# Kernel tuning notes

Measured on AMD Instinct MI355X. Metric: run time of the kernel, lower is better.

Reference implementation:

```python
import jax, jax.numpy as jnp
import numpy as np

S, V, H = 32, 16, 8            # hidden_scalars, hidden_vectors, num_heads
N, E = 10000, 100000           # nodes, edges
NRB, RH = 16, 64               # radial basis, radial MLP hidden
TH = S + 3 * V                 # packed irreps width (80)
WNUM = S * S + V * S + S * V + 2 * V * V  # TP weight_numel = 2560


def setup_inputs() -> dict:
    key = jax.random.key(0)
    ks = jax.random.split(key, 16)
    inp = {}
    inp["node_features"] = jax.random.normal(ks[0], (N, TH), jnp.float32)
    inp["edge_index"] = jax.random.randint(ks[1], (2, E), 0, N)
    inp["edge_sh"] = jax.random.normal(ks[2], (E, 4), jnp.float32)
    inp["edge_radial"] = jax.random.uniform(ks[3], (E, NRB), dtype=jnp.float32)
    inp["edge_envelope"] = jax.random.uniform(ks[4], (E,), dtype=jnp.float32)
    # radial MLP
    inp["W1"] = jax.random.normal(ks[5], (NRB, RH), jnp.float32) / np.sqrt(NRB)
    inp["b1"] = jnp.zeros((RH,), jnp.float32)
    inp["W2"] = jax.random.normal(ks[6], (RH, WNUM), jnp.float32) / np.sqrt(RH)
    inp["b2"] = jnp.zeros((WNUM,), jnp.float32)
    # attention query/key nets (scalar channels only)
    inp["Wq"] = jax.random.normal(ks[7], (S, H), jnp.float32) / np.sqrt(S)
    inp["bq"] = jnp.zeros((H,), jnp.float32)
    inp["Wk"] = jax.random.normal(ks[8], (S, H), jnp.float32) / np.sqrt(S)
    inp["bk"] = jnp.zeros((H,), jnp.float32)
    # equivariant linears (per-irrep channel mixing, e3nn style, no bias)
    inp["Wout_s"] = jax.random.normal(ks[9], (S, S), jnp.float32)
    inp["Wout_v"] = jax.random.normal(ks[10], (V, V), jnp.float32)
    inp["Wg_s"] = jax.random.normal(ks[11], (S, S + V), jnp.float32)
    inp["Wg_v"] = jax.random.normal(ks[12], (V, V), jnp.float32)
    # equivariant batch norm params
    inp["bn_ws"] = jnp.ones((S,), jnp.float32)
    inp["bn_bs"] = jnp.zeros((S,), jnp.float32)
    inp["bn_wv"] = jnp.ones((V,), jnp.float32)
    return inp


def _forward(node_features, edge_sh, edge_radial, edge_envelope,
             W1, b1, W2, b2, Wq, bq, Wk, bk,
             Wout_s, Wout_v, Wg_s, Wg_v, bn_ws, bn_bs, bn_wv, src, dst):
    # --- per-edge TP weights from radial MLP -> (E, WNUM), the big tensor ---
    tp_w = jax.nn.silu(edge_radial @ W1 + b1) @ W2 + b2
    offs = np.cumsum([0, S * S, V * S, S * V, V * V, V * V])
    WA = tp_w[:, offs[0]:offs[1]].reshape(-1, S, S)  # 0e x 0e -> 0e
    WB = tp_w[:, offs[1]:offs[2]].reshape(-1, V, S)  # 1o x 1o -> 0e
    WC = tp_w[:, offs[2]:offs[3]].reshape(-1, S, V)  # 0e x 1o -> 1o
    WD = tp_w[:, offs[3]:offs[4]].reshape(-1, V, V)  # 1o x 0e -> 1o
    WE = tp_w[:, offs[4]:offs[5]].reshape(-1, V, V)  # 1o x 1o -> 1o (cross)

    # --- gather source features, split irreps ---
    s_src = node_features[src, :S]                       # (E, S)
    v_src = node_features[src, S:].reshape(-1, V, 3)     # (E, V, 3)
    y0 = edge_sh[:, 0:1]                                 # (E, 1) l=0
    y1 = edge_sh[:, 1:4]                                 # (E, 3) l=1

    a0 = 1.0 / np.sqrt(S + V)       # path normalization, 0e output
    a1 = 1.0 / np.sqrt(S + 2 * V)   # path normalization, 1o output

    dot = (v_src * y1[:, None, :]).sum(-1) / np.sqrt(3.0)          # (E, V)
    msg_s = a0 * (jnp.einsum('es,esk->ek', s_src * y0, WA)
                  + jnp.einsum('ev,evk->ek', dot, WB))             # (E, S)
    crs = jnp.cross(v_src, y1[:, None, :]) / np.sqrt(2.0)          # (E, V, 3)
    msg_v = a1 * (jnp.einsum('es,ec,esk->ekc', s_src, y1, WC)
                  + jnp.einsum('evc,evk->ekc', v_src * y0[:, :, None], WD)
                  + jnp.einsum('evc,evk->ekc', crs, WE))           # (E, V, 3)
    messages = jnp.concatenate([msg_s, msg_v.reshape(-1, 3 * V)], axis=-1)

    # --- scatter-softmax attention over incoming edges per destination ---
    q = node_features[dst, :S] @ Wq + bq                 # (E, H)
    k = msg_s @ Wk + bk                                  # (E, H)
    logits = (q * k).sum(-1) / np.sqrt(H) + jnp.log(edge_envelope + 1e-8)
    mx = jax.ops.segment_max(logits, dst, num_segments=N)
    ex = jnp.exp(logits - mx[dst])
    den = jax.ops.segment_sum(ex, dst, num_segments=N)
    attn = ex / (den[dst] + 1e-8)                        # (E,)

    agg = jax.ops.segment_sum(attn[:, None] * messages, dst, num_segments=N)

    # --- equivariant output linear ---
    agg_s = agg[:, :S] @ Wout_s / np.sqrt(S)
    agg_v = jnp.einsum('nvc,vw->nwc', agg[:, S:].reshape(-1, V, 3), Wout_v) / np.sqrt(V)

    # --- gate ---
    gs = agg_s @ Wg_s / np.sqrt(S)                       # (N, S+V)
    gv = jnp.einsum('nvc,vw->nwc', agg_v, Wg_v) / np.sqrt(V)
    s = jax.nn.silu(gs[:, :S])
    g = jax.nn.sigmoid(gs[:, S:])
    v = g[:, :, None] * gv
    act = jnp.concatenate([s, v.reshape(-1, 3 * V)], axis=-1)

    # --- residual + equivariant batch norm ---
    x = act + node_features
    xs = x[:, :S]
    xv = x[:, S:].reshape(-1, V, 3)
    mean = xs.mean(0)
    var = xs.var(0)
    xs = (xs - mean) / jnp.sqrt(var + 1e-5) * bn_ws + bn_bs
    vn = (xv * xv).mean(-1).mean(0)                      # (V,) component norm
    xv = xv * (bn_wv / jnp.sqrt(vn + 1e-5))[None, :, None]
    return jnp.concatenate([xs, xv.reshape(-1, 3 * V)], axis=-1)


def reference(node_features, edge_index, edge_sh, edge_radial, edge_envelope,
              W1, b1, W2, b2, Wq, bq, Wk, bk,
              Wout_s, Wout_v, Wg_s, Wg_v, bn_ws, bn_bs, bn_wv):
    src, dst = edge_index[0], edge_index[1]
    return _forward(node_features, edge_sh, edge_radial, edge_envelope,
                    W1, b1, W2, b2, Wq, bq, Wk, bk,
                    Wout_s, Wout_v, Wg_s, Wg_v, bn_ws, bn_bs, bn_wv, src, dst)
```

## Files before the change

### kernel.cpp

```cpp
#include <hip/hip_runtime.h>
#include <math.h>

typedef __bf16 bf16x8 __attribute__((ext_vector_type(8)));
typedef __bf16 bf16x4 __attribute__((ext_vector_type(4)));
typedef float  f32x4  __attribute__((ext_vector_type(4)));
typedef float  f32x2  __attribute__((ext_vector_type(2)));
typedef unsigned long long u64x2 __attribute__((ext_vector_type(2)));

__device__ __forceinline__ float silu_f(float x){ return x / (1.f + __expf(-x)); }
__device__ __forceinline__ float sigm_f(float x){ return 1.f / (1.f + __expf(-x)); }

__device__ __forceinline__ float ntld_f(const float* p){
  return __builtin_nontemporal_load(p);
}
__device__ __forceinline__ float ntbf(const __bf16* p){
  unsigned short us = __builtin_nontemporal_load((const unsigned short*)p);
  union { unsigned u; float f; } cv; cv.u = ((unsigned)us) << 16;
  return cv.f;
}
__device__ __forceinline__ void nt_store_f(float* p, float v){
  __builtin_nontemporal_store(v, p);
}
__device__ __forceinline__ void nt_store_b8(__bf16* p, bf16x8 v){
  u64x2 u; __builtin_memcpy(&u, &v, 16);
// ... 142 lines not shown
  for (int i = t; i < 5120; i += 256){
    int e = i / 80, idx = i - e*80;
    featT[idx][e] = nf[(size_t)src_l[e]*80 + idx];
  }
  for (int i = t; i < 4096; i += 256){
    int e = i & 63, h = i >> 6;
    float acc = b1l[h];
    #pragma unroll
    for (int r = 0; r < 16; ++r) acc += radl[e][r]*w1l[r*64+h];
    u_l[e][h] = (__bf16)silu_f(acc);
  }
  __syncthreads();

  const float inv_s3 = 0.57735026918962576f;
  const float inv_s2 = 0.70710678118654752f;
  const float a0 = 0.14433756729740643f;
  const float a1 = 0.125f;

  for (int i = t; i < 3072; i += 256){
    int r = i >> 6, e = i & 63;
    float val;
    if (r < 32) val = a0 * shlT[0][e] * featT[r][e];
    else {
      int v = r - 32;
      float dot = (featT[32+v*3][e]*shlT[1][e] + featT[33+v*3][e]*shlT[2][e]
                 + featT[34+v*3][e]*shlT[3][e]) * inv_s3;
      val = a0 * dot;
    }
    cab_l[r][e] = (__bf16)val;
  }
  for (int i = t; i < 12288; i += 256){
    int e = i & 63, r = (i >> 6) & 63, c = i >> 12;
    float val;
    if (r < 32) val = a1 * shlT[1+c][e] * featT[r][e];
    else if (r < 48){
      int v = r - 32;
      val = a1 * shlT[0][e] * featT[32+v*3+c][e];
    } else {
      int v = r - 48;
      int c1 = c+1; if (c1 > 2) c1 -= 3;
      int c2 = c+2; if (c2 > 2) c2 -= 3;
      val = a1 * inv_s2 * (featT[32+v*3+c1][e]*shlT[1+c2][e]
                         - featT[32+v*3+c2][e]*shlT[1+c1][e]);
    }
    cv_l[r][c][e] = (__bf16)val;
  }
  __syncthreads();

  for (int i = t; i < 512; i += 256){
    int tl = i >> 7, rem = i & 127, k8 = rem >> 4, e = rem & 15;
    if (tg0 + tl < NT){
      bf16x8 v = *(const bf16x8*)&u_l[tl*16 + e][k8*8];
      *(bf16x8*)((char*)uG + (size_t)(tg0+tl)*2048 + k8*256 + e*16) = v;
    }
  }
  for (int i = t; i < 384; i += 256){
    int tl = i / 96, rem = i - tl*96, r = rem >> 1, h = rem & 1;
    if (tg0 + tl < NT){
      bf16x8 v = *(const bf16x8*)&cab_l[r][tl*16 + h*8];
      *(bf16x8*)((char*)cabG + (size_t)(tg0+tl)*1536 + r*32 + h*16) = v;
    }
  }
  for (int i = t; i < 1536; i += 256){
    int tl = i / 384, rem = i - tl*384, r = rem / 6, rem2 = rem - r*6,
        c = rem2 >> 1, h = rem2 & 1;
    if (tg0 + tl < NT){
      bf16x8 v = *(const bf16x8*)&cv_l[r][c][tl*16 + h*8];
      *(bf16x8*)((char*)cvG + (size_t)(tg0+tl)*6144 + r*96 + c*32 + h*16) = v;
    }
  }
}

#define LOAD_PANEL(BASE_IT, NITS) do {                                         \
    for (int idx = t; idx < (NITS)*128; idx += 512){                           \
      int itl_ = idx >> 7, rem_ = idx & 127, half_ = rem_ >> 6, r6_ = rem_ & 63;\
      int col_ = r6_ >> 2, quad_ = r6_ & 3;                                    \
      *(float4*)(panel + itl_*2048 + half_*1024 + quad_*256 + col_*16) =       \
        *(const float4*)(w2b + half_*163840 + (size_t)((BASE_IT)+itl_)*1024    \
                         + col_*64 + quad_*16);                                \
    }                                                                          \
    for (int i = t; i < (NITS)*16; i += 512) b2l[i] = b2[(BASE_IT)*16 + i];    \
  } while(0)

#define S_PHASE(SECOND) do {                                                   \
  for (int outer = 0; outer < 2; ++outer){                                     \
    const int tgA = 2*wgid + outer*4096;                                       \
    if (tgA >= NT) break;                                                      \
    const int tgB = tgA + 1;                                                   \
    const bool hB = (tgB < NT);                                                \
    const int tgBc = hB ? tgB : tgA;                                           \
    bf16x8 aA0 = *(const bf16x8*)(uGb + (size_t)tgA*2048 + uOff);              \
    bf16x8 aA1 = *(const bf16x8*)(uGb + (size_t)tgA*2048 + 1024 + uOff);       \
    bf16x8 aB0 = *(const bf16x8*)(uGb + (size_t)tgBc*2048 + uOff);             \
    bf16x8 aB1 = *(const bf16x8*)(uGb + (size_t)tgBc*2048 + 1024 + uOff);      \
    {                                                                          \
      bf16x8 cA16 = *(const bf16x8*)(cabGb + (size_t)tgA*1536 + lane*16);      \
      bf16x4 cA8  = *(const bf16x4*)(cabGb + (size_t)tgA*1536 + 1024 + lane*8);\
      bf16x8 cB16 = *(const bf16x8*)(cabGb + (size_t)tgBc*1536 + lane*16);     \
      bf16x4 cB8  = *(const bf16x4*)(cabGb + (size_t)tgBc*1536 + 1024 + lane*8);\
      *(bf16x8*)(myCab + lane*16) = cA16;                                      \
      *(bf16x4*)(myCab + 1024 + lane*8) = cA8;                                 \
      *(bf16x8*)(myCab + 1536 + lane*16) = cB16;                               \
      *(bf16x4*)(myCab + 2560 + lane*8) = cB8;                                 \
    }                                                                          \
    f32x2 sA0lo={0,0}, sA0hi={0,0}, sA1lo={0,0}, sA1hi={0,0};                  \
    f32x2 sB0lo={0,0}, sB0hi={0,0}, sB1lo={0,0}, sB1hi={0,0};                  \
    if (SECOND){                                                               \
      f32x4 p;                                                                 \
      p = *(const f32x4*)(partU + (size_t)tgA*768 + lane*8);                   \
      sA0lo[0]=p[0]; sA0lo[1]=p[1]; sA0hi[0]=p[2]; sA0hi[1]=p[3];              \
      p = *(const f32x4*)(partU + (size_t)tgA*768 + lane*8 + 4);               \
      sA1lo[0]=p[0]; sA1lo[1]=p[1]; sA1hi[0]=p[2]; sA1hi[1]=p[3];              \
      p = *(const f32x4*)(partU + (size_t)tgBc*768 + lane*8);                  \
      sB0lo[0]=p[0]; sB0lo[1]=p[1]; sB0hi[0]=p[2]; sB0hi[1]=p[3];              \
      p = *(const f32x4*)(partU + (size_t)tgBc*768 + lane*8 + 4);              \
      sB1lo[0]=p[0]; sB1lo[1]=p[1]; sB1hi[0]=p[2]; sB1hi[1]=p[3];              \
    }                                                                          \
    _Pragma("unroll 4")                                                        \
    for (int itl = 0; itl < 48; ++itl){                                        \
      bf16x8 B0 = *(const bf16x8*)(panel + itl*2048 + laneOff);                \
      bf16x8 B1 = *(const bf16x8*)(panel + itl*2048 + 1024 + laneOff);         \
      f32x4 dA; dA[0]=0;dA[1]=0;dA[2]=0;dA[3]=0; f32x4 dB = dA;                \
      dA = __builtin_amdgcn_mfma_f32_16x16x32_bf16(aA0, B0, dA, 0,0,0);        \
      dB = __builtin_amdgcn_mfma_f32_16x16x32_bf16(aB0, B0, dB, 0,0,0);        \
      dA = __builtin_amdgcn_mfma_f32_16x16x32_bf16(aA1, B1, dA, 0,0,0);        \
      dB = __builtin_amdgcn_mfma_f32_16x16x32_bf16(aB1, B1, dB, 0,0,0);        \
      const float bias = b2l[itl*16 + nlo];                                    \
      f32x2 bb; bb[0]=bias; bb[1]=bias;                                        \
      f32x2 dAlo = __builtin_shufflevector(dA,dA,0,1) + bb;                    \
      f32x2 dAhi = __builtin_shufflevector(dA,dA,2,3) + bb;                    \
      f32x2 dBlo = __builtin_shufflevector(dB,dB,0,1) + bb;                    \
      f32x2 dBhi = __builtin_shufflevector(dB,dB,2,3) + bb;                    \
      const int r = (SECOND)*24 + (itl>>1);                                    \
      bf16x4 cA = *(const bf16x4*)(myCab + r*32 + quad*8);                     \
      bf16x4 cB = *(const bf16x4*)(myCab + 1536 + r*32 + quad*8);              \
      if (itl & 1){                                                            \
        sA1lo += b4lo(cA)*dAlo; sA1hi += b4hi(cA)*dAhi;                        \
        sB1lo += b4lo(cB)*dBlo; sB1hi += b4hi(cB)*dBhi;                        \
      } else {                                                                 \
        sA0lo += b4lo(cA)*dAlo; sA0hi += b4hi(cA)*dAhi;                        \
        sB0lo += b4lo(cB)*dBlo; sB0hi += b4hi(cB)*dBhi;                        \
      }                                                                        \
    }                                                                          \
    if (!(SECOND)){                                                            \
      f32x4 P;                                                                 \
      P[0]=sA0lo[0]; P[1]=sA0lo[1]; P[2]=sA0hi[0]; P[3]=sA0hi[1];              \
      *(f32x4*)(partU + (size_t)tgA*768 + lane*8) = P;                         \
      P[0]=sA1lo[0]; P[1]=sA1lo[1]; P[2]=sA1hi[0]; P[3]=sA1hi[1];              \
      *(f32x4*)(partU + (size_t)tgA*768 + lane*8 + 4) = P;                     \
      if (hB){                                                                 \
        P[0]=sB0lo[0]; P[1]=sB0lo[1]; P[2]=sB0hi[0]; P[3]=sB0hi[1];            \
        *(f32x4*)(partU + (size_t)tgB*768 + lane*8) = P;                       \
        P[0]=sB1lo[0]; P[1]=sB1lo[1]; P[2]=sB1hi[0]; P[3]=sB1hi[1];            \
        *(f32x4*)(partU + (size_t)tgB*768 + lane*8 + 4) = P;                   \
      }                                                                        \
    } else {                                                                   \
      const int eb = quad*4;                                                   \
      S_FLUSH(tgA, sA0lo, sA0hi, sA1lo, sA1hi);                                \
      if (hB){ S_FLUSH(tgB, sB0lo, sB0hi, sB1lo, sB1hi); }                     \
    }                                                                          \
  }                                                                            \
} while(0)

#define S_FLUSH(TG, S0LO, S0HI, S1LO, S1HI) do {                               \
      myOut[(eb+0)*56 + nlo] = S0LO[0];                                        \
      myOut[(eb+1)*56 + nlo] = S0LO[1];                                        \
      myOut[(eb+2)*56 + nlo] = S0HI[0];                                        \
      myOut[(eb+3)*56 + nlo] = S0HI[1];                                        \
      myOut[(eb+0)*56 + 16+nlo] = S1LO[0];                                     \
      myOut[(eb+1)*56 + 16+nlo] = S1LO[1];                                     \
      myOut[(eb+2)*56 + 16+nlo] = S1HI[0];                                     \
      myOut[(eb+3)*56 + 16+nlo] = S1HI[1];                                     \
      const int e0e = (TG)*16;                                                 \
      { int e = lane>>2, seg = lane&3, eg = e0e + e;                           \
        if (eg < E){                                                           \
          f32x4 m0 = *(const f32x4*)&myOut[e*56 + seg*8];                      \
          f32x4 m1 = *(const f32x4*)&myOut[e*56 + seg*8 + 4];                  \
          bf16x8 o; o[0]=(__bf16)m0[0]; o[1]=(__bf16)m0[1];                    \
          o[2]=(__bf16)m0[2]; o[3]=(__bf16)m0[3]; o[4]=(__bf16)m1[0];          \
          o[5]=(__bf16)m1[1]; o[6]=(__bf16)m1[2]; o[7]=(__bf16)m1[3];          \
          nt_store_b8(msgs + (size_t)permG[eg]*80 + seg*8, o);                 \
        } }                                                                    \
      for (int r8 = 0; r8 < 2; ++r8){                                          \
        int e = r8*8 + (lane>>3), kq = lane&7, eg = e0e + e;                   \
        f32x4 ms = *(const f32x4*)&myOut[e*56 + kq*4];                         \
        int dn = ei[(size_t)E + min(eg, E-1)];                                 \
        const float* kvp = kvt + (size_t)dn*32 + kq*4;                         \
        float part = ms[0]*kvp[0]+ms[1]*kvp[1]+ms[2]*kvp[2]+ms[3]*kvp[3];      \
        part += __shfl_xor(part, 1);                                           \
        part += __shfl_xor(part, 2);                                           \
        part += __shfl_xor(part, 4);                                           \
        if (kq == 0 && eg < E){                                                \
          float lg = (part + carr[dn]) * 0.35355339059327373f                  \
                   + logf(ntld_f(&env[eg]) + 1e-8f);                           \
          nt_store_f(&logits_s[permG[eg]], lg);                                \
        } }                                                                    \
  } while(0)

#define V_FLUSH(TG, V0LO, V0HI, V1LO, V1HI, V2LO, V2HI) do {                   \
      const int cb2 = nlo*3;                                                   \
      myOut[(eb+0)*56 + cb2+0] = V0LO[0];                                      \
      myOut[(eb+1)*56 + cb2+0] = V0LO[1];                                      \
      myOut[(eb+2)*56 + cb2+0] = V0HI[0];                                      \
      myOut[(eb+3)*56 + cb2+0] = V0HI[1];                                      \
      myOut[(eb+0)*56 + cb2+1] = V1LO[0];                                      \
      myOut[(eb+1)*56 + cb2+1] = V1LO[1];                                      \
      myOut[(eb+2)*56 + cb2+1] = V1HI[0];                                      \
      myOut[(eb+3)*56 + cb2+1] = V1HI[1];                                      \
      myOut[(eb+0)*56 + cb2+2] = V2LO[0];                                      \
      myOut[(eb+1)*56 + cb2+2] = V2LO[1];                                      \
      myOut[(eb+2)*56 + cb2+2] = V2HI[0];                                      \
      myOut[(eb+3)*56 + cb2+2] = V2HI[1];                                      \
      const int e0e = (TG)*16;                                                 \
      for (int i = lane; i < 96; i += 64){                                     \
        int e = i/6, seg = i - (i/6)*6, eg = e0e + e;                          \
        if (eg < E){                                                           \
          f32x4 m0 = *(const f32x4*)&myOut[e*56 + seg*8];                      \
          f32x4 m1 = *(const f32x4*)&myOut[e*56 + seg*8 + 4];                  \
          bf16x8 o; o[0]=(__bf16)m0[0]; o[1]=(__bf16)m0[1];                    \
          o[2]=(__bf16)m0[2]; o[3]=(__bf16)m0[3]; o[4]=(__bf16)m1[0];          \
          o[5]=(__bf16)m1[1]; o[6]=(__bf16)m1[2]; o[7]=(__bf16)m1[3];          \
          nt_store_b8(msgs + (size_t)permG[eg]*80 + 32 + seg*8, o);            \
        } }                                                                    \
  } while(0)

#define V_PHASE(SECOND) do {                                                   \
  for (int outer = 0; outer < 2; ++outer){                                     \
    const int tgA = 2*wgid + outer*4096;                                       \
    if (tgA >= NT) break;                                                      \
    const int tgB = tgA + 1;                                                   \
    const bool hB = (tgB < NT);                                                \
    const int tgBc = hB ? tgB : tgA;                                           \
    bf16x8 aA0 = *(const bf16x8*)(uGb + (size_t)tgA*2048 + uOff);              \
    bf16x8 aA1 = *(const bf16x8*)(uGb + (size_t)tgA*2048 + 1024 + uOff);       \
    bf16x8 aB0 = *(const bf16x8*)(uGb + (size_t)tgBc*2048 + uOff);             \
    bf16x8 aB1 = *(const bf16x8*)(uGb + (size_t)tgBc*2048 + 1024 + uOff);      \
    {                                                                          \
      bf16x8 c0 = *(const bf16x8*)(cvGb + (size_t)tgA*6144 + (SECOND)*3072 + lane*48);\
      bf16x8 c1 = *(const bf16x8*)(cvGb + (size_t)tgA*6144 + (SECOND)*3072 + lane*48 + 16);\
      bf16x8 c2 = *(const bf16x8*)(cvGb + (size_t)tgA*6144 + (SECOND)*3072 + lane*48 + 32);\
      *(bf16x8*)(myCab + lane*48)      = c0;                                   \
      *(bf16x8*)(myCab + lane*48 + 16) = c1;                                   \
      *(bf16x8*)(myCab + lane*48 + 32) = c2;                                   \
      c0 = *(const bf16x8*)(cvGb + (size_t)tgBc*6144 + (SECOND)*3072 + lane*48);\
      c1 = *(const bf16x8*)(cvGb + (size_t)tgBc*6144 + (SECOND)*3072 + lane*48 + 16);\
      c2 = *(const bf16x8*)(cvGb + (size_t)tgBc*6144 + (SECOND)*3072 + lane*48 + 32);\
      *(bf16x8*)(myCab + 3072 + lane*48)      = c0;                            \
      *(bf16x8*)(myCab + 3072 + lane*48 + 16) = c1;                            \
      *(bf16x8*)(myCab + 3072 + lane*48 + 32) = c2;                            \
    }                                                                          \
    f32x2 vA0lo={0,0}, vA0hi={0,0}, vA1lo={0,0}, vA1hi={0,0}, vA2lo={0,0}, vA2hi={0,0};\
    f32x2 vB0lo={0,0}, vB0hi={0,0}, vB1lo={0,0}, vB1hi={0,0}, vB2lo={0,0}, vB2hi={0,0};\
    if (SECOND){                                                               \
      f32x4 p;                                                                 \
      p = *(const f32x4*)(partU + (size_t)tgA*768 + lane*12);                  \
      vA0lo[0]=p[0]; vA0lo[1]=p[1]; vA0hi[0]=p[2]; vA0hi[1]=p[3];              \
      p = *(const f32x4*)(partU + (size_t)tgA*768 + lane*12 + 4);              \
      vA1lo[0]=p[0]; vA1lo[1]=p[1]; vA1hi[0]=p[2]; vA1hi[1]=p[3];              \
      p = *(const f32x4*)(partU + (size_t)tgA*768 + lane*12 + 8);              \
      vA2lo[0]=p[0]; vA2lo[1]=p[1]; vA2hi[0]=p[2]; vA2hi[1]=p[3];              \
      p = *(const f32x4*)(partU + (size_t)tgBc*768 + lane*12);                 \
      vB0lo[0]=p[0]; vB0lo[1]=p[1]; vB0hi[0]=p[2]; vB0hi[1]=p[3];              \
      p = *(const f32x4*)(partU + (size_t)tgBc*768 + lane*12 + 4);             \
      vB1lo[0]=p[0]; vB1lo[1]=p[1]; vB1hi[0]=p[2]; vB1hi[1]=p[3];              \
      p = *(const f32x4*)(partU + (size_t)tgBc*768 + lane*12 + 8);             \
      vB2lo[0]=p[0]; vB2lo[1]=p[1]; vB2hi[0]=p[2]; vB2hi[1]=p[3];              \
    }                                                                          \
    _Pragma("unroll 4")                                                        \
    for (int itl = 0; itl < 32; ++itl){                                        \
      bf16x8 B0 = *(const bf16x8*)(panel + itl*2048 + laneOff);                \
      bf16x8 B1 = *(const bf16x8*)(panel + itl*2048 + 1024 + laneOff);         \
      f32x4 dA; dA[0]=0;dA[1]=0;dA[2]=0;dA[3]=0; f32x4 dB = dA;                \
      dA = __builtin_amdgcn_mfma_f32_16x16x32_bf16(aA0, B0, dA, 0,0,0);        \
      dB = __builtin_amdgcn_mfma_f32_16x16x32_bf16(aB0, B0, dB, 0,0,0);        \
      dA = __builtin_amdgcn_mfma_f32_16x16x32_bf16(aA1, B1, dA, 0,0,0);        \
      dB = __builtin_amdgcn_mfma_f32_16x16x32_bf16(aB1, B1, dB, 0,0,0);        \
      const float bias = b2l[itl*16 + nlo];                                    \
      f32x2 bb; bb[0]=bias; bb[1]=bias;                                        \
      f32x2 dAlo = __builtin_shufflevector(dA,dA,0,1) + bb;                    \
      f32x2 dAhi = __builtin_shufflevector(dA,dA,2,3) + bb;                    \
      f32x2 dBlo = __builtin_shufflevector(dB,dB,0,1) + bb;                    \
      f32x2 dBhi = __builtin_shufflevector(dB,dB,2,3) + bb;                    \
      const char* cbA_ = myCab + itl*96;                                       \
      const char* cbB_ = myCab + 3072 + itl*96;                                \
      bf16x4 q0 = *(const bf16x4*)(cbA_ + quad*8);                             \
      bf16x4 q1 = *(const bf16x4*)(cbA_ + 32 + quad*8);                        \
      bf16x4 q2 = *(const bf16x4*)(cbA_ + 64 + quad*8);                        \
      vA0lo += b4lo(q0)*dAlo; vA0hi += b4hi(q0)*dAhi;                          \
      vA1lo += b4lo(q1)*dAlo; vA1hi += b4hi(q1)*dAhi;                          \
      vA2lo += b4lo(q2)*dAlo; vA2hi += b4hi(q2)*dAhi;                          \
      q0 = *(const bf16x4*)(cbB_ + quad*8);                                    \
      q1 = *(const bf16x4*)(cbB_ + 32 + quad*8);                               \
      q2 = *(const bf16x4*)(cbB_ + 64 + quad*8);                               \
      vB0lo += b4lo(q0)*dBlo; vB0hi += b4hi(q0)*dBhi;                          \
      vB1lo += b4lo(q1)*dBlo; vB1hi += b4hi(q1)*dBhi;                          \
      vB2lo += b4lo(q2)*dBlo; vB2hi += b4hi(q2)*dBhi;                          \
    }                                                                          \
    if (!(SECOND)){                                                            \
      f32x4 P;                                                                 \
      P[0]=vA0lo[0]; P[1]=vA0lo[1]; P[2]=vA0hi[0]; P[3]=vA0hi[1];              \
      *(f32x4*)(partU + (size_t)tgA*768 + lane*12) = P;                        \
      P[0]=vA1lo[0]; P[1]=vA1lo[1]; P[2]=vA1hi[0]; P[3]=vA1hi[1];              \
      *(f32x4*)(partU + (size_t)tgA*768 + lane*12 + 4) = P;                    \
      P[0]=vA2lo[0]; P[1]=vA2lo[1]; P[2]=vA2hi[0]; P[3]=vA2hi[1];              \
      *(f32x4*)(partU + (size_t)tgA*768 + lane*12 + 8) = P;                    \
      if (hB){                                                                 \
        P[0]=vB0lo[0]; P[1]=vB0lo[1]; P[2]=vB0hi[0]; P[3]=vB0hi[1];            \
        *(f32x4*)(partU + (size_t)tgB*768 + lane*12) = P;                      \
        P[0]=vB1lo[0]; P[1]=vB1lo[1]; P[2]=vB1hi[0]; P[3]=vB1hi[1];            \
        *(f32x4*)(partU + (size_t)tgB*768 + lane*12 + 4) = P;                  \
        P[0]=vB2lo[0]; P[1]=vB2lo[1]; P[2]=vB2hi[0]; P[3]=vB2hi[1];            \
        *(f32x4*)(partU + (size_t)tgB*768 + lane*12 + 8) = P;                  \
      }                                                                        \
    } else {                                                                   \
      const int eb = quad*4;                                                   \
      V_FLUSH(tgA, vA0lo, vA0hi, vA1lo, vA1hi, vA2lo, vA2hi);                  \
      if (hB){ V_FLUSH(tgB, vB0lo, vB0hi, vB1lo, vB1hi, vB2lo, vB2hi); }       \
    }                                                                          \
  }                                                                            \
} while(0)

__global__ void __launch_bounds__(512, 1) k_edge(
    const __bf16* __restrict__ W2t, const float* __restrict__ b2,
    const __bf16* __restrict__ uG, const __bf16* __restrict__ cabG,
    const __bf16* __restrict__ cvG, const int* __restrict__ ei,
    const int* __restrict__ permG, const float* __restrict__ kvt,
    const float* __restrict__ carr, const float* __restrict__ env,
    float* __restrict__ partU, __bf16* __restrict__ msgs,
    float* __restrict__ logits_s, int E, int NT)
{
  __shared__ __align__(16) char panel[98304];
  __shared__ __align__(16) char wstage[8][6144];
  __shared__ float b2l[768];

  const int t = threadIdx.x;
  const int lane = t & 63;
  const int wv   = t >> 6;
  const int quad = lane >> 4;
  const int nlo  = lane & 15;
  const int wgid = blockIdx.x*8 + wv;
  const int laneOff = quad*256 + nlo*16;
  const int uOff    = quad*256 + nlo*16;
  char*  myCab = wstage[wv];
  float* myOut = (float*)wstage[wv];
  const char* w2b   = (const char*)W2t;
  const char* uGb   = (const char*)uG;
  const char* cabGb = (const char*)cabG;
  const char* cvGb  = (const char*)cvG;

  LOAD_PANEL(0, 48);
  __syncthreads();
  S_PHASE(0);
  __syncthreads();
  LOAD_PANEL(48, 48);
  __syncthreads();
  S_PHASE(1);
  __syncthreads();
  LOAD_PANEL(96, 32);
  __syncthreads();
  V_PHASE(0);
  __syncthreads();
  LOAD_PANEL(128, 32);
  __syncthreads();
  V_PHASE(1);
}

__global__ void __launch_bounds__(256) k_agg(
    const __bf16* __restrict__ msgs, const float* __restrict__ logits_s,
    const int* __restrict__ cursor, const float* __restrict__ nf,
    const float* __restrict__ Wout_s, const float* __restrict__ Wout_v,
    const float* __restrict__ Wg_s, const float* __restrict__ Wg_v,
    float* __restrict__ xbuf, float* __restrict__ bnacc, int N)
{
  __shared__ float aggl[4][80];
  __shared__ float t1[4][96];
  __shared__ float t2[4][96];
  __shared__ float bnl[80];
  const int t = threadIdx.x, l = t & 63, wv = t >> 6;
  const int n = blockIdx.x*4 + wv;
  const bool act = (n < N);
  const int nc = act ? n : (N-1);
  if (t < 80) bnl[t] = 0.f;

  const int r0 = (nc == 0) ? 0 : cursor[nc-1];
  const int r1 = cursor[nc];
  const int deg = act ? (r1 - r0) : 0;

  float mym = -3.4e38f;
  for (int i = l; i < deg; i += 64) mym = fmaxf(mym, logits_s[r0+i]);
  #pragma unroll
  for (int s = 32; s; s >>= 1) mym = fmaxf(mym, __shfl_xor(mym, s));
  float denp = 0.f, acc0 = 0.f, acc1 = 0.f;
  for (int c0 = 0; c0 < deg; c0 += 64){
    const int len = min(64, deg - c0);
    float ex = 0.f;
    if (l < len) ex = __expf(logits_s[r0+c0+l] - mym);
    denp += ex;
    for (int j0 = 0; j0 < len; j0 += 4){
      const int jn = len - j0;
      const __bf16* base = msgs + (size_t)(r0+c0+j0)*80;
      float v0=0,v1=0,v2=0,v3=0, w0=0,w1=0,w2=0,w3=0;
      float a0_=0,a1_=0,a2_=0,a3_=0;
      v0 = ntbf(&base[l]); if (l < 16) w0 = ntbf(&base[64+l]); a0_ = __shfl(ex, j0);
      if (jn > 1){ v1 = ntbf(&base[80+l]);  if (l < 16) w1 = ntbf(&base[144+l]); a1_ = __shfl(ex, j0+1); }
      if (jn > 2){ v2 = ntbf(&base[160+l]); if (l < 16) w2 = ntbf(&base[224+l]); a2_ = __shfl(ex, j0+2); }
      if (jn > 3){ v3 = ntbf(&base[240+l]); if (l < 16) w3 = ntbf(&base[304+l]); a3_ = __shfl(ex, j0+3); }
      acc0 += a0_*v0 + a1_*v1 + a2_*v2 + a3_*v3;
      if (l < 16) acc1 += a0_*w0 + a1_*w1 + a2_*w2 + a3_*w3;
    }
  }
  #pragma unroll
  for (int s = 32; s; s >>= 1) denp += __shfl_xor(denp, s);
  const float inv = 1.f/(denp + 1e-8f);
  aggl[wv][l] = acc0 * inv;
  if (l < 16) aggl[wv][64+l] = acc1 * inv;
  __syncthreads();

  const float* arow = &aggl[wv][0];
  const float iS = 0.17677669529663687f;
  const float iV = 0.25f;
  for (int o = l; o < 80; o += 64){
    float val = 0.f;
    if (o < 32){
      for (int s = 0; s < 32; ++s) val += arow[s]*Wout_s[s*32+o];
      val *= iS;
    } else {
      int w = (o-32)/3, c = (o-32)-w*3;
      for (int v = 0; v < 16; ++v) val += arow[32+v*3+c]*Wout_v[v*16+w];
      val *= iV;
    }
    t1[wv][o] = val;
  }
  __syncthreads();
  for (int o = l; o < 96; o += 64){
    float val = 0.f;
    if (o < 48){
      for (int k = 0; k < 32; ++k) val += t1[wv][k]*Wg_s[k*48+o];
      val *= iS;
    } else {
      int w = (o-48)/3, c = (o-48)-w*3;
      for (int v = 0; v < 16; ++v) val += t1[wv][32+v*3+c]*Wg_v[v*16+w];
      val *= iV;
    }
    t2[wv][o] = val;
  }
  __syncthreads();
  for (int o = l; o < 80; o += 64){
// ... 6 lines not shown
        atomicAdd(&bnl[32+o], x*x);
      }
    } else {
      int w = (o-32)/3;
      x = sigm_f(t2[wv][32+w]) * t2[wv][48+(o-32)] + nf[(size_t)nc*80+o];
      if (act){
        nt_store_f(&xbuf[(size_t)n*80+o], x);
        atomicAdd(&bnl[64+w], x*x);
      }
    }
  }
  __syncthreads();
  if (t < 80) atomicAdd(&bnacc[t], bnl[t]);
}

__global__ void __launch_bounds__(256) k_out(const float* __restrict__ xbuf,
    const float* __restrict__ bnacc,
    const float* __restrict__ bn_ws, const float* __restrict__ bn_bs,
    const float* __restrict__ bn_wv, float* __restrict__ out, int N){
  __shared__ float coef[80];
  int t = threadIdx.x;
  float fN = (float)N;
  if (t < 32){
    float mean = bnacc[t]/fN;
    float var = bnacc[32+t]/fN - mean*mean;
    float cm = bn_ws[t]*rsqrtf(var + 1e-5f);
    coef[t] = cm;
    coef[32+t] = bn_bs[t] - mean*cm;
  } else if (t < 48){
    int v = t - 32;
    coef[64+v] = bn_wv[v]*rsqrtf(bnacc[64+v]/(3.f*fN) + 1e-5f);
  }
  __syncthreads();
  int i = blockIdx.x*256 + t;
  if (i >= N*80) return;
  int o = i - (i/80)*80;
  float x = ntld_f(&xbuf[i]);
  nt_store_f(&out[i], (o < 32) ? (x*coef[o] + coef[32+o]) : (x*coef[64+(o-32)/3]));
}

extern "C" void kernel_launch(void* const* d_in, const int* in_sizes, int n_in,
                              void* d_out, int out_size, void* d_ws, size_t ws_size,
                              hipStream_t stream) {
  const float* nf     = (const float*)d_in[0];
  const int*   ei     = (const int*)  d_in[1];
  const float* sh     = (const float*)d_in[2];
  const float* radial = (const float*)d_in[3];
  const float* env    = (const float*)d_in[4];
  const float* W1     = (const float*)d_in[5];
  const float* b1     = (const float*)d_in[6];
  const float* W2     = (const float*)d_in[7];
  const float* b2     = (const float*)d_in[8];
  const float* Wq     = (const float*)d_in[9];
  const float* bq     = (const float*)d_in[10];
  const float* Wk     = (const float*)d_in[11];
  const float* bk     = (const float*)d_in[12];
  const float* Wout_s = (const float*)d_in[13];
  const float* Wout_v = (const float*)d_in[14];
  const float* Wg_s   = (const float*)d_in[15];
  const float* Wg_v   = (const float*)d_in[16];
  const float* bn_ws  = (const float*)d_in[17];
  const float* bn_bs  = (const float*)d_in[18];
  const float* bn_wv  = (const float*)d_in[19];

  const int E = in_sizes[4];
  const int N = in_sizes[0] / 80;
  const int NT = (E + 15)/16;

  float* ws = (float*)d_ws;
  size_t off = 0;
  __bf16* w2t    = (__bf16*)(ws + off); off += 81920;
  __bf16* msgs   = (__bf16*)(ws + off); off += (size_t)E*40;
  float* logits_s= ws + off; off += E;
  int* cnt       = (int*)(ws + off); off += N;
  int* cursor    = (int*)(ws + off); off += N;
  float* xbuf    = ws + off; off += (size_t)N*80;
  float* bnacc   = ws + off; off += 80;
  float* kvt     = ws + off; off += (size_t)N*32;
  float* carr    = ws + off; off += N;
  int* permG     = (int*)(ws + off); off += E;
  __bf16* uG     = (__bf16*)(ws + off); off += (size_t)NT*512;
  __bf16* cabG   = (__bf16*)(ws + off); off += (size_t)NT*384;
  __bf16* cvG    = (__bf16*)(ws + off); off += (size_t)NT*1536;
  float* partU   = ws + off; off += (size_t)NT*768;

  hipMemsetAsync(cnt, 0, (size_t)N*sizeof(int), stream);

  const int nbPrep = 640;
  const int nbHist = (E + 255)/256;
  const int nbKv   = (N + 63)/64;
  k_setup<<<nbPrep + nbHist + nbKv, 256, 0, stream>>>(W2, w2t, ei, cnt,
      nf, Wq, bq, Wk, bk, kvt, carr, nbPrep, nbHist, N, E);
  k_scan<<<1, 1024, 0, stream>>>(cnt, cursor, bnacc, N, E);
  k_prep<<<(E + 63)/64, 256, 0, stream>>>(nf, ei, sh, radial, W1, b1, cursor,
      uG, cabG, cvG, permG, E, NT);
  k_edge<<<256, 512, 0, stream>>>(w2t, b2, uG, cabG, cvG, ei, permG,
      kvt, carr, env, partU, msgs, logits_s, E, NT);
  k_agg<<<(N + 3)/4, 256, 0, stream>>>(msgs, logits_s, cursor, nf,
      Wout_s, Wout_v, Wg_s, Wg_v, xbuf, bnacc, N);
  k_out<<<(N*80 + 255)/256, 256, 0, stream>>>(xbuf, bnacc, bn_ws, bn_bs, bn_wv,
      (float*)d_out, N);
}
```

Baseline: 361.0 us.

## Keep edge-tile accumulators in registers across panel phases, drop partU spill

Each wave now holds the A operands and scalar/vector accumulators for all four of its edge tiles in registers for the whole kernel. The global partU round-trip between the first and second W2 panel halves is gone, along with the repeated uG loads. Tile assignment changes from adjacent pairs to strided tiles (wgid, +2048, +4096, +6144), and the cab/cv staging buffers are laid out per tile. The cost is much higher register pressure under launch_bounds(512,1), which may cause spills. The wstage buffer is also reused for staging while flushes happen, so correct ordering depends on the flush macros.

```diff
diff --git a/kernel.cpp b/kernel.cpp
--- a/kernel.cpp
+++ b/kernel.cpp
@@ -248,85 +248,83 @@
     for (int i = t; i < (NITS)*16; i += 512) b2l[i] = b2[(BASE_IT)*16 + i];    \
   } while(0)
 
-#define S_PHASE(SECOND) do {                                                   \
-  for (int outer = 0; outer < 2; ++outer){                                     \
-    const int tgA = 2*wgid + outer*4096;                                       \
-    if (tgA >= NT) break;                                                      \
-    const int tgB = tgA + 1;                                                   \
-    const bool hB = (tgB < NT);                                                \
-    const int tgBc = hB ? tgB : tgA;                                           \
-    bf16x8 aA0 = *(const bf16x8*)(uGb + (size_t)tgA*2048 + uOff);              \
-    bf16x8 aA1 = *(const bf16x8*)(uGb + (size_t)tgA*2048 + 1024 + uOff);       \
-    bf16x8 aB0 = *(const bf16x8*)(uGb + (size_t)tgBc*2048 + uOff);             \
-    bf16x8 aB1 = *(const bf16x8*)(uGb + (size_t)tgBc*2048 + 1024 + uOff);      \
-    {                                                                          \
-      bf16x8 cA16 = *(const bf16x8*)(cabGb + (size_t)tgA*1536 + lane*16);      \
-      bf16x4 cA8  = *(const bf16x4*)(cabGb + (size_t)tgA*1536 + 1024 + lane*8);\
-      bf16x8 cB16 = *(const bf16x8*)(cabGb + (size_t)tgBc*1536 + lane*16);     \
-      bf16x4 cB8  = *(const bf16x4*)(cabGb + (size_t)tgBc*1536 + 1024 + lane*8);\
-      *(bf16x8*)(myCab + lane*16) = cA16;                                      \
-      *(bf16x4*)(myCab + 1024 + lane*8) = cA8;                                 \
-      *(bf16x8*)(myCab + 1536 + lane*16) = cB16;                               \
-      *(bf16x4*)(myCab + 2560 + lane*8) = cB8;                                 \
-    }                                                                          \
-    f32x2 sA0lo={0,0}, sA0hi={0,0}, sA1lo={0,0}, sA1hi={0,0};                  \
-    f32x2 sB0lo={0,0}, sB0hi={0,0}, sB1lo={0,0}, sB1hi={0,0};                  \
-    if (SECOND){                                                               \
-      f32x4 p;                                                                 \
-      p = *(const f32x4*)(partU + (size_t)tgA*768 + lane*8);                   \
-      sA0lo[0]=p[0]; sA0lo[1]=p[1]; sA0hi[0]=p[2]; sA0hi[1]=p[3];              \
-      p = *(const f32x4*)(partU + (size_t)tgA*768 + lane*8 + 4);               \
-      sA1lo[0]=p[0]; sA1lo[1]=p[1]; sA1hi[0]=p[2]; sA1hi[1]=p[3];              \
-      p = *(const f32x4*)(partU + (size_t)tgBc*768 + lane*8);                  \
-      sB0lo[0]=p[0]; sB0lo[1]=p[1]; sB0hi[0]=p[2]; sB0hi[1]=p[3];              \
-      p = *(const f32x4*)(partU + (size_t)tgBc*768 + lane*8 + 4);              \
-      sB1lo[0]=p[0]; sB1lo[1]=p[1]; sB1hi[0]=p[2]; sB1hi[1]=p[3];              \
-    }                                                                          \
+#define CAB_STAGE(TGC, BASE) do {                                              \
+    bf16x8 x_ = *(const bf16x8*)(cabGb + (size_t)(TGC)*1536 + lane*16);        \
+    bf16x4 y_ = *(const bf16x4*)(cabGb + (size_t)(TGC)*1536 + 1024 + lane*8);  \
+    *(bf16x8*)(myCab + (BASE) + lane*16) = x_;                                 \
+    *(bf16x4*)(myCab + (BASE) + 1024 + lane*8) = y_;                           \
+  } while(0)
+
+#define CV_STAGE(TGC, BASE, HALF) do {                                         \
+    bf16x8 c0_ = *(const bf16x8*)(cvGb + (size_t)(TGC)*6144 + (HALF)*3072 + lane*48);\
+    bf16x8 c1_ = *(const bf16x8*)(cvGb + (size_t)(TGC)*6144 + (HALF)*3072 + lane*48 + 16);\
+    bf16x8 c2_ = *(const bf16x8*)(cvGb + (size_t)(TGC)*6144 + (HALF)*3072 + lane*48 + 32);\
+    *(bf16x8*)(myCab + (BASE) + lane*48)      = c0_;                           \
+    *(bf16x8*)(myCab + (BASE) + lane*48 + 16) = c1_;                           \
+    *(bf16x8*)(myCab + (BASE) + lane*48 + 32) = c2_;                           \
+  } while(0)
+
+#define S_PAIR(SECOND, CBA, CBB, TA, TB) do {                                  \
     _Pragma("unroll 4")                                                        \
     for (int itl = 0; itl < 48; ++itl){                                        \
-      bf16x8 B0 = *(const bf16x8*)(panel + itl*2048 + laneOff);                \
-      bf16x8 B1 = *(const bf16x8*)(panel + itl*2048 + 1024 + laneOff);         \
-      f32x4 dA; dA[0]=0;dA[1]=0;dA[2]=0;dA[3]=0; f32x4 dB = dA;                \
-      dA = __builtin_amdgcn_mfma_f32_16x16x32_bf16(aA0, B0, dA, 0,0,0);        \
-      dB = __builtin_amdgcn_mfma_f32_16x16x32_bf16(aB0, B0, dB, 0,0,0);        \
-      dA = __builtin_amdgcn_mfma_f32_16x16x32_bf16(aA1, B1, dA, 0,0,0);        \
-      dB = __builtin_amdgcn_mfma_f32_16x16x32_bf16(aB1, B1, dB, 0,0,0);        \
-      const float bias = b2l[itl*16 + nlo];                                    \
-      f32x2 bb; bb[0]=bias; bb[1]=bias;                                        \
-      f32x2 dAlo = __builtin_shufflevector(dA,dA,0,1) + bb;                    \
-      f32x2 dAhi = __builtin_shufflevector(dA,dA,2,3) + bb;                    \
-      f32x2 dBlo = __builtin_shufflevector(dB,dB,0,1) + bb;                    \
-      f32x2 dBhi = __builtin_shufflevector(dB,dB,2,3) + bb;                    \
-      const int r = (SECOND)*24 + (itl>>1);                                    \
-      bf16x4 cA = *(const bf16x4*)(myCab + r*32 + quad*8);                     \
-      bf16x4 cB = *(const bf16x4*)(myCab + 1536 + r*32 + quad*8);              \
+      bf16x8 B0_ = *(const bf16x8*)(panel + itl*2048 + laneOff);               \
+      bf16x8 B1_ = *(const bf16x8*)(panel + itl*2048 + 1024 + laneOff);        \
+      f32x4 dA_; dA_[0]=0;dA_[1]=0;dA_[2]=0;dA_[3]=0; f32x4 dB_ = dA_;         \
+      dA_ = __builtin_amdgcn_mfma_f32_16x16x32_bf16(u##TA##_0, B0_, dA_, 0,0,0);\
+      dB_ = __builtin_amdgcn_mfma_f32_16x16x32_bf16(u##TB##_0, B0_, dB_, 0,0,0);\
+      dA_ = __builtin_amdgcn_mfma_f32_16x16x32_bf16(u##TA##_1, B1_, dA_, 0,0,0);\
+      dB_ = __builtin_amdgcn_mfma_f32_16x16x32_bf16(u##TB##_1, B1_, dB_, 0,0,0);\
+      const float bias_ = b2l[itl*16 + nlo];                                   \
+      f32x2 bb_; bb_[0]=bias_; bb_[1]=bias_;                                   \
+      f32x2 dAlo_ = __builtin_shufflevector(dA_,dA_,0,1) + bb_;                \
+      f32x2 dAhi_ = __builtin_shufflevector(dA_,dA_,2,3) + bb_;                \
+      f32x2 dBlo_ = __builtin_shufflevector(dB_,dB_,0,1) + bb_;                \
+      f32x2 dBhi_ = __builtin_shufflevector(dB_,dB_,2,3) + bb_;                \
+      const int r_ = (SECOND)*24 + (itl>>1);                                   \
+      bf16x4 cA_ = *(const bf16x4*)(myCab + (CBA) + r_*32 + quad*8);           \
+      bf16x4 cB_ = *(const bf16x4*)(myCab + (CBB) + r_*32 + quad*8);           \
       if (itl & 1){                                                            \
-        sA1lo += b4lo(cA)*dAlo; sA1hi += b4hi(cA)*dAhi;                        \
-        sB1lo += b4lo(cB)*dBlo; sB1hi += b4hi(cB)*dBhi;                        \
+        s1l##TA += b4lo(cA_)*dAlo_; s1h##TA += b4hi(cA_)*dAhi_;                \
+        s1l##TB += b4lo(cB_)*dBlo_; s1h##TB += b4hi(cB_)*dBhi_;                \
       } else {                                                                 \
-        sA0lo += b4lo(cA)*dAlo; sA0hi += b4hi(cA)*dAhi;                        \
-        sB0lo += b4lo(cB)*dBlo; sB0hi += b4hi(cB)*dBhi;                        \
+        s0l##TA += b4lo(cA_)*dAlo_; s0h##TA += b4hi(cA_)*dAhi_;                \
+        s0l##TB += b4lo(cB_)*dBlo_; s0h##TB += b4hi(cB_)*dBhi_;                \
       }                                                                        \
     }                                                                          \
-    if (!(SECOND)){                                                            \
-      f32x4 P;                                                                 \
-      P[0]=sA0lo[0]; P[1]=sA0lo[1]; P[2]=sA0hi[0]; P[3]=sA0hi[1];              \
-      *(f32x4*)(partU + (size_t)tgA*768 + lane*8) = P;                         \
-      P[0]=sA1lo[0]; P[1]=sA1lo[1]; P[2]=sA1hi[0]; P[3]=sA1hi[1];              \
-      *(f32x4*)(partU + (size_t)tgA*768 + lane*8 + 4) = P;                     \
-      if (hB){                                                                 \
-        P[0]=sB0lo[0]; P[1]=sB0lo[1]; P[2]=sB0hi[0]; P[3]=sB0hi[1];            \
-        *(f32x4*)(partU + (size_t)tgB*768 + lane*8) = P;                       \
-        P[0]=sB1lo[0]; P[1]=sB1lo[1]; P[2]=sB1hi[0]; P[3]=sB1hi[1];            \
-        *(f32x4*)(partU + (size_t)tgB*768 + lane*8 + 4) = P;                   \
-      }                                                                        \
-    } else {                                                                   \
-      const int eb = quad*4;                                                   \
-      S_FLUSH(tgA, sA0lo, sA0hi, sA1lo, sA1hi);                                \
-      if (hB){ S_FLUSH(tgB, sB0lo, sB0hi, sB1lo, sB1hi); }                     \
+  } while(0)
+
+#define V_PAIR(TA, TB) do {                                                    \
+    _Pragma("unroll 4")                                                        \
+    for (int itl = 0; itl < 32; ++itl){                                        \
+      bf16x8 B0_ = *(const bf16x8*)(panel + itl*2048 + laneOff);               \
+      bf16x8 B1_ = *(const bf16x8*)(panel + itl*2048 + 1024 + laneOff);        \
+      f32x4 dA_; dA_[0]=0;dA_[1]=0;dA_[2]=0;dA_[3]=0; f32x4 dB_ = dA_;         \
+      dA_ = __builtin_amdgcn_mfma_f32_16x16x32_bf16(u##TA##_0, B0_, dA_, 0,0,0);\
+      dB_ = __builtin_amdgcn_mfma_f32_16x16x32_bf16(u##TB##_0, B0_, dB_, 0,0,0);\
+      dA_ = __builtin_amdgcn_mfma_f32_16x16x32_bf16(u##TA##_1, B1_, dA_, 0,0,0);\
+      dB_ = __builtin_amdgcn_mfma_f32_16x16x32_bf16(u##TB##_1, B1_, dB_, 0,0,0);\
+      const float bias_ = b2l[itl*16 + nlo];                                   \
+      f32x2 bb_; bb_[0]=bias_; bb_[1]=bias_;                                   \
+      f32x2 dAlo_ = __builtin_shufflevector(dA_,dA_,0,1) + bb_;                \
+      f32x2 dAhi_ = __builtin_shufflevector(dA_,dA_,2,3) + bb_;                \
+      f32x2 dBlo_ = __builtin_shufflevector(dB_,dB_,0,1) + bb_;                \
+      f32x2 dBhi_ = __builtin_shufflevector(dB_,dB_,2,3) + bb_;                \
+      const char* cbA_ = myCab + itl*96;                                       \
+      const char* cbB_ = myCab + 3072 + itl*96;                                \
+      bf16x4 q0_ = *(const bf16x4*)(cbA_ + quad*8);                            \
+      bf16x4 q1_ = *(const bf16x4*)(cbA_ + 32 + quad*8);                       \
+      bf16x4 q2_ = *(const bf16x4*)(cbA_ + 64 + quad*8);                       \
+      v0l##TA += b4lo(q0_)*dAlo_; v0h##TA += b4hi(q0_)*dAhi_;                  \
+      v1l##TA += b4lo(q1_)*dAlo_; v1h##TA += b4hi(q1_)*dAhi_;                  \
+      v2l##TA += b4lo(q2_)*dAlo_; v2h##TA += b4hi(q2_)*dAhi_;                  \
+      q0_ = *(const bf16x4*)(cbB_ + quad*8);                                   \
+      q1_ = *(const bf16x4*)(cbB_ + 32 + quad*8);                              \
+      q2_ = *(const bf16x4*)(cbB_ + 64 + quad*8);                              \
+      v0l##TB += b4lo(q0_)*dBlo_; v0h##TB += b4hi(q0_)*dBhi_;                  \
+      v1l##TB += b4lo(q1_)*dBlo_; v1h##TB += b4hi(q1_)*dBhi_;                  \
+      v2l##TB += b4lo(q2_)*dBlo_; v2h##TB += b4hi(q2_)*dBhi_;                  \
     }                                                                          \
-  }                                                                            \
-} while(0)
+  } while(0)
 
 #define S_FLUSH(TG, S0LO, S0HI, S1LO, S1HI) do {                               \
       myOut[(eb+0)*56 + nlo] = S0LO[0];                                        \
@@ -390,110 +388,13 @@
         } }                                                                    \
   } while(0)
 
-#define V_PHASE(SECOND) do {                                                   \
-  for (int outer = 0; outer < 2; ++outer){                                     \
-    const int tgA = 2*wgid + outer*4096;                                       \
-    if (tgA >= NT) break;                                                      \
-    const int tgB = tgA + 1;                                                   \
-    const bool hB = (tgB < NT);                                                \
-    const int tgBc = hB ? tgB : tgA;                                           \
-    bf16x8 aA0 = *(const bf16x8*)(uGb + (size_t)tgA*2048 + uOff);              \
-    bf16x8 aA1 = *(const bf16x8*)(uGb + (size_t)tgA*2048 + 1024 + uOff);       \
-    bf16x8 aB0 = *(const bf16x8*)(uGb + (size_t)tgBc*2048 + uOff);             \
-    bf16x8 aB1 = *(const bf16x8*)(uGb + (size_t)tgBc*2048 + 1024 + uOff);      \
-    {                                                                          \
-      bf16x8 c0 = *(const bf16x8*)(cvGb + (size_t)tgA*6144 + (SECOND)*3072 + lane*48);\
-      bf16x8 c1 = *(const bf16x8*)(cvGb + (size_t)tgA*6144 + (SECOND)*3072 + lane*48 + 16);\
-      bf16x8 c2 = *(const bf16x8*)(cvGb + (size_t)tgA*6144 + (SECOND)*3072 + lane*48 + 32);\
-      *(bf16x8*)(myCab + lane*48)      = c0;                                   \
-      *(bf16x8*)(myCab + lane*48 + 16) = c1;                                   \
-      *(bf16x8*)(myCab + lane*48 + 32) = c2;                                   \
-      c0 = *(const bf16x8*)(cvGb + (size_t)tgBc*6144 + (SECOND)*3072 + lane*48);\
-      c1 = *(const bf16x8*)(cvGb + (size_t)tgBc*6144 + (SECOND)*3072 + lane*48 + 16);\
-      c2 = *(const bf16x8*)(cvGb + (size_t)tgBc*6144 + (SECOND)*3072 + lane*48 + 32);\
-      *(bf16x8*)(myCab + 3072 + lane*48)      = c0;                            \
-      *(bf16x8*)(myCab + 3072 + lane*48 + 16) = c1;                            \
-      *(bf16x8*)(myCab + 3072 + lane*48 + 32) = c2;                            \
-    }                                                                          \
-    f32x2 vA0lo={0,0}, vA0hi={0,0}, vA1lo={0,0}, vA1hi={0,0}, vA2lo={0,0}, vA2hi={0,0};\
-    f32x2 vB0lo={0,0}, vB0hi={0,0}, vB1lo={0,0}, vB1hi={0,0}, vB2lo={0,0}, vB2hi={0,0};\
-    if (SECOND){                                                               \
-      f32x4 p;                                                                 \
-      p = *(const f32x4*)(partU + (size_t)tgA*768 + lane*12);                  \
-      vA0lo[0]=p[0]; vA0lo[1]=p[1]; vA0hi[0]=p[2]; vA0hi[1]=p[3];              \
-      p = *(const f32x4*)(partU + (size_t)tgA*768 + lane*12 + 4);              \
-      vA1lo[0]=p[0]; vA1lo[1]=p[1]; vA1hi[0]=p[2]; vA1hi[1]=p[3];              \
-      p = *(const f32x4*)(partU + (size_t)tgA*768 + lane*12 + 8);              \
-      vA2lo[0]=p[0]; vA2lo[1]=p[1]; vA2hi[0]=p[2]; vA2hi[1]=p[3];              \
-      p = *(const f32x4*)(partU + (size_t)tgBc*768 + lane*12);                 \
-      vB0lo[0]=p[0]; vB0lo[1]=p[1]; vB0hi[0]=p[2]; vB0hi[1]=p[3];              \
-      p = *(const f32x4*)(partU + (size_t)tgBc*768 + lane*12 + 4);             \
-      vB1lo[0]=p[0]; vB1lo[1]=p[1]; vB1hi[0]=p[2]; vB1hi[1]=p[3];              \
-      p = *(const f32x4*)(partU + (size_t)tgBc*768 + lane*12 + 8);             \
-      vB2lo[0]=p[0]; vB2lo[1]=p[1]; vB2hi[0]=p[2]; vB2hi[1]=p[3];              \
-    }                                                                          \
-    _Pragma("unroll 4")                                                        \
-    for (int itl = 0; itl < 32; ++itl){                                        \
-      bf16x8 B0 = *(const bf16x8*)(panel + itl*2048 + laneOff);                \
-      bf16x8 B1 = *(const bf16x8*)(panel + itl*2048 + 1024 + laneOff);         \
-      f32x4 dA; dA[0]=0;dA[1]=0;dA[2]=0;dA[3]=0; f32x4 dB = dA;                \
-      dA = __builtin_amdgcn_mfma_f32_16x16x32_bf16(aA0, B0, dA, 0,0,0);        \
-      dB = __builtin_amdgcn_mfma_f32_16x16x32_bf16(aB0, B0, dB, 0,0,0);        \
-      dA = __builtin_amdgcn_mfma_f32_16x16x32_bf16(aA1, B1, dA, 0,0,0);        \
-      dB = __builtin_amdgcn_mfma_f32_16x16x32_bf16(aB1, B1, dB, 0,0,0);        \
-      const float bias = b2l[itl*16 + nlo];                                    \
-      f32x2 bb; bb[0]=bias; bb[1]=bias;                                        \
-      f32x2 dAlo = __builtin_shufflevector(dA,dA,0,1) + bb;                    \
-      f32x2 dAhi = __builtin_shufflevector(dA,dA,2,3) + bb;                    \
-      f32x2 dBlo = __builtin_shufflevector(dB,dB,0,1) + bb;                    \
-      f32x2 dBhi = __builtin_shufflevector(dB,dB,2,3) + bb;                    \
-      const char* cbA_ = myCab + itl*96;                                       \
-      const char* cbB_ = myCab + 3072 + itl*96;                                \
-      bf16x4 q0 = *(const bf16x4*)(cbA_ + quad*8);                             \
-      bf16x4 q1 = *(const bf16x4*)(cbA_ + 32 + quad*8);                        \
-      bf16x4 q2 = *(const bf16x4*)(cbA_ + 64 + quad*8);                        \
-      vA0lo += b4lo(q0)*dAlo; vA0hi += b4hi(q0)*dAhi;                          \
-      vA1lo += b4lo(q1)*dAlo; vA1hi += b4hi(q1)*dAhi;                          \
-      vA2lo += b4lo(q2)*dAlo; vA2hi += b4hi(q2)*dAhi;                          \
-      q0 = *(const bf16x4*)(cbB_ + quad*8);                                    \
-      q1 = *(const bf16x4*)(cbB_ + 32 + quad*8);                               \
-      q2 = *(const bf16x4*)(cbB_ + 64 + quad*8);                               \
-      vB0lo += b4lo(q0)*dBlo; vB0hi += b4hi(q0)*dBhi;                          \
-      vB1lo += b4lo(q1)*dBlo; vB1hi += b4hi(q1)*dBhi;                          \
-      vB2lo += b4lo(q2)*dBlo; vB2hi += b4hi(q2)*dBhi;                          \
-    }                                                                          \
-    if (!(SECOND)){                                                            \
-      f32x4 P;                                                                 \
-      P[0]=vA0lo[0]; P[1]=vA0lo[1]; P[2]=vA0hi[0]; P[3]=vA0hi[1];              \
-      *(f32x4*)(partU + (size_t)tgA*768 + lane*12) = P;                        \
-      P[0]=vA1lo[0]; P[1]=vA1lo[1]; P[2]=vA1hi[0]; P[3]=vA1hi[1];              \
-      *(f32x4*)(partU + (size_t)tgA*768 + lane*12 + 4) = P;                    \
-      P[0]=vA2lo[0]; P[1]=vA2lo[1]; P[2]=vA2hi[0]; P[3]=vA2hi[1];              \
-      *(f32x4*)(partU + (size_t)tgA*768 + lane*12 + 8) = P;                    \
-      if (hB){                                                                 \
-        P[0]=vB0lo[0]; P[1]=vB0lo[1]; P[2]=vB0hi[0]; P[3]=vB0hi[1];            \
-        *(f32x4*)(partU + (size_t)tgB*768 + lane*12) = P;                      \
-        P[0]=vB1lo[0]; P[1]=vB1lo[1]; P[2]=vB1hi[0]; P[3]=vB1hi[1];            \
-        *(f32x4*)(partU + (size_t)tgB*768 + lane*12 + 4) = P;                  \
-        P[0]=vB2lo[0]; P[1]=vB2lo[1]; P[2]=vB2hi[0]; P[3]=vB2hi[1];            \
-        *(f32x4*)(partU + (size_t)tgB*768 + lane*12 + 8) = P;                  \
-      }                                                                        \
-    } else {                                                                   \
-      const int eb = quad*4;                                                   \
-      V_FLUSH(tgA, vA0lo, vA0hi, vA1lo, vA1hi, vA2lo, vA2hi);                  \
-      if (hB){ V_FLUSH(tgB, vB0lo, vB0hi, vB1lo, vB1hi, vB2lo, vB2hi); }       \
-    }                                                                          \
-  }                                                                            \
-} while(0)
-
 __global__ void __launch_bounds__(512, 1) k_edge(
     const __bf16* __restrict__ W2t, const float* __restrict__ b2,
     const __bf16* __restrict__ uG, const __bf16* __restrict__ cabG,
     const __bf16* __restrict__ cvG, const int* __restrict__ ei,
     const int* __restrict__ permG, const float* __restrict__ kvt,
     const float* __restrict__ carr, const float* __restrict__ env,
-    float* __restrict__ partU, __bf16* __restrict__ msgs,
-    float* __restrict__ logits_s, int E, int NT)
+    __bf16* __restrict__ msgs, float* __restrict__ logits_s, int E, int NT)
 {
   __shared__ __align__(16) char panel[98304];
   __shared__ __align__(16) char wstage[8][6144];
@@ -514,21 +415,65 @@
   const char* cabGb = (const char*)cabG;
   const char* cvGb  = (const char*)cvG;
 
+  const int tA0 = wgid, tB0 = wgid + 2048, tA1 = wgid + 4096, tB1 = wgid + 6144;
+  const bool hA0 = tA0 < NT, hB0 = tB0 < NT, hA1 = tA1 < NT, hB1 = tB1 < NT;
+  const int cA0 = min(tA0, NT-1), cB0 = min(tB0, NT-1);
+  const int cA1 = min(tA1, NT-1), cB1 = min(tB1, NT-1);
+
+  const bf16x8 uA0_0 = *(const bf16x8*)(uGb + (size_t)cA0*2048 + uOff);
+  const bf16x8 uA0_1 = *(const bf16x8*)(uGb + (size_t)cA0*2048 + 1024 + uOff);
+  const bf16x8 uB0_0 = *(const bf16x8*)(uGb + (size_t)cB0*2048 + uOff);
+  const bf16x8 uB0_1 = *(const bf16x8*)(uGb + (size_t)cB0*2048 + 1024 + uOff);
+  const bf16x8 uA1_0 = *(const bf16x8*)(uGb + (size_t)cA1*2048 + uOff);
+  const bf16x8 uA1_1 = *(const bf16x8*)(uGb + (size_t)cA1*2048 + 1024 + uOff);
+  const bf16x8 uB1_0 = *(const bf16x8*)(uGb + (size_t)cB1*2048 + uOff);
+  const bf16x8 uB1_1 = *(const bf16x8*)(uGb + (size_t)cB1*2048 + 1024 + uOff);
+
+  f32x2 s0lA0={0,0}, s0hA0={0,0}, s1lA0={0,0}, s1hA0={0,0};
+  f32x2 s0lB0={0,0}, s0hB0={0,0}, s1lB0={0,0}, s1hB0={0,0};
+  f32x2 s0lA1={0,0}, s0hA1={0,0}, s1lA1={0,0}, s1hA1={0,0};
+  f32x2 s0lB1={0,0}, s0hB1={0,0}, s1lB1={0,0}, s1hB1={0,0};
+
+  const int eb = quad*4;
+
   LOAD_PANEL(0, 48);
-  __syncthreads();
-  S_PHASE(0);
+  CAB_STAGE(cA0, 0); CAB_STAGE(cB0, 1536); CAB_STAGE(cA1, 3072); CAB_STAGE(cB1, 4608);
+  __syncthreads();
+  S_PAIR(0, 0, 1536, A0, B0);
+  S_PAIR(0, 3072, 4608, A1, B1);
   __syncthreads();
   LOAD_PANEL(48, 48);
   __syncthreads();
-  S_PHASE(1);
-  __syncthreads();
+  S_PAIR(1, 0, 1536, A0, B0);
+  S_PAIR(1, 3072, 4608, A1, B1);
+  if (hA0) S_FLUSH(tA0, s0lA0, s0hA0, s1lA0, s1hA0);
+  if (hB0) S_FLUSH(tB0, s0lB0, s0hB0, s1lB0, s1hB0);
+  if (hA1) S_FLUSH(tA1, s0lA1, s0hA1, s1lA1, s1hA1);
+  if (hB1) S_FLUSH(tB1, s0lB1, s0hB1, s1lB1, s1hB1);
+  __syncthreads();
+
+  f32x2 v0lA0={0,0}, v0hA0={0,0}, v1lA0={0,0}, v1hA0={0,0}, v2lA0={0,0}, v2hA0={0,0};
+  f32x2 v0lB0={0,0}, v0hB0={0,0}, v1lB0={0,0}, v1hB0={0,0}, v2lB0={0,0}, v2hB0={0,0};
+  f32x2 v0lA1={0,0}, v0hA1={0,0}, v1lA1={0,0}, v1hA1={0,0}, v2lA1={0,0}, v2hA1={0,0};
+  f32x2 v0lB1={0,0}, v0hB1={0,0}, v1lB1={0,0}, v1hB1={0,0}, v2lB1={0,0}, v2hB1={0,0};
+
   LOAD_PANEL(96, 32);
-  __syncthreads();
-  V_PHASE(0);
+  CV_STAGE(cA0, 0, 0); CV_STAGE(cB0, 3072, 0);
+  __syncthreads();
+  V_PAIR(A0, B0);
+  CV_STAGE(cA1, 0, 0); CV_STAGE(cB1, 3072, 0);
+  V_PAIR(A1, B1);
   __syncthreads();
   LOAD_PANEL(128, 32);
-  __syncthreads();
-  V_PHASE(1);
+  CV_STAGE(cA0, 0, 1); CV_STAGE(cB0, 3072, 1);
+  __syncthreads();
+  V_PAIR(A0, B0);
+  CV_STAGE(cA1, 0, 1); CV_STAGE(cB1, 3072, 1);
+  V_PAIR(A1, B1);
+  if (hA0) V_FLUSH(tA0, v0lA0, v0hA0, v1lA0, v1hA0, v2lA0, v2hA0);
+  if (hB0) V_FLUSH(tB0, v0lB0, v0hB0, v1lB0, v1hB0, v2lB0, v2hB0);
+  if (hA1) V_FLUSH(tA1, v0lA1, v0hA1, v1lA1, v1hA1, v2lA1, v2hA1);
+  if (hB1) V_FLUSH(tB1, v0lB1, v0hB1, v1lB1, v1hB1, v2lB1, v2hB1);
 }
 
 __global__ void __launch_bounds__(256) k_agg(
@@ -701,7 +646,6 @@
   __bf16* uG     = (__bf16*)(ws + off); off += (size_t)NT*512;
   __bf16* cabG   = (__bf16*)(ws + off); off += (size_t)NT*384;
   __bf16* cvG    = (__bf16*)(ws + off); off += (size_t)NT*1536;
-  float* partU   = ws + off; off += (size_t)NT*768;
 
   hipMemsetAsync(cnt, 0, (size_t)N*sizeof(int), stream);
 
@@ -714,7 +658,7 @@
   k_prep<<<(E + 63)/64, 256, 0, stream>>>(nf, ei, sh, radial, W1, b1, cursor,
       uG, cabG, cvG, permG, E, NT);
   k_edge<<<256, 512, 0, stream>>>(w2t, b2, uG, cabG, cvG, ei, permG,
-      kvt, carr, env, partU, msgs, logits_s, E, NT);
+      kvt, carr, env, msgs, logits_s, E, NT);
   k_agg<<<(N + 3)/4, 256, 0, stream>>>(msgs, logits_s, cursor, nf,
       Wout_s, Wout_v, Wg_s, Wg_v, xbuf, bnacc, N);
   k_out<<<(N*80 + 255)/256, 256, 0, stream>>>(xbuf, bnacc, bn_ws, bn_bs, bn_wv,
```

Measured after the change: 361.1 us. About the same (+0.0%).
